# Performance work log

Measured on AMD Instinct MI355X. Metric: run time of the kernel, lower is better.

The kernel has to match this reference:

```python
import jax, jax.numpy as jnp
import numpy as np

# Constants from the source's eval path
BBOX_STDS = (0.1, 0.1, 0.2, 0.2)   # cfg.TRAIN.BBOX_NORMALIZE_STDS (MEANS are zeros)
PRE_NMS = 300                       # cfg.TEST.RPN_POST_NMS_TOP_N
POST_K = 100                        # cfg.PERSON_NMS (fixed output size; zero-padded)
NMS_THRESH = 0.3
SCORE_THRESH = 0.05


def setup_inputs() -> dict:
    key = jax.random.key(0)
    k1, k2, k3, k4 = jax.random.split(key, 4)
    B, N = 64, 32768
    H = W = 1024.0
    # plausible RPN proposal boxes inside the image
    xy = jax.random.uniform(k1, (B, N, 2)) * (W - 160.0)
    wh = jax.random.uniform(k2, (B, N, 2)) * 120.0 + 8.0
    boxes = jnp.concatenate([xy, xy + wh], axis=-1)          # [B,N,4] x1y1x2y2
    cls_prob = jax.random.uniform(k3, (B, N, 2))              # softmax probs [bg, person]
    box_deltas = jax.random.normal(k4, (B, N, 4)) * 0.5
    im_info = jnp.tile(jnp.array([H, W, 1.0], jnp.float32), (B, 1))
    return {"cls_prob": cls_prob, "boxes": boxes, "box_deltas": box_deltas, "im_info": im_info}


def _decode_and_clip(boxes, deltas, im_info):
    # bbox_transform_inv with de-normalized deltas, then clip_boxes
    stds = jnp.array(BBOX_STDS, boxes.dtype)
    d = deltas * stds                                         # MEANS are zero
    w = boxes[..., 2] - boxes[..., 0] + 1.0
    h = boxes[..., 3] - boxes[..., 1] + 1.0
    cx = boxes[..., 0] + 0.5 * w
    cy = boxes[..., 1] + 0.5 * h
    pcx = d[..., 0] * w + cx
    pcy = d[..., 1] * h + cy
    pw = jnp.exp(d[..., 2]) * w
    ph = jnp.exp(d[..., 3]) * h
    x1 = pcx - 0.5 * pw
    y1 = pcy - 0.5 * ph
    x2 = pcx + 0.5 * pw
    y2 = pcy + 0.5 * ph
    hmax = im_info[:, 0][:, None] - 1.0   # [B,1]
    wmax = im_info[:, 1][:, None] - 1.0
    x1 = jnp.clip(x1, 0.0, wmax)
    y1 = jnp.clip(y1, 0.0, hmax)
    x2 = jnp.clip(x2, 0.0, wmax)
    y2 = jnp.clip(y2, 0.0, hmax)
    return jnp.stack([x1, y1, x2, y2], axis=-1)               # [B,N,4]


def _nms_single(boxes_i, scores_i):
    # threshold -> sort (top-k) -> greedy NMS -> fixed-size padded output
    valid = scores_i >= SCORE_THRESH
    s = jnp.where(valid, scores_i, -jnp.inf)
    topv, topi = jax.lax.top_k(s, PRE_NMS)                    # descending sort + pre_nms_topN
    b = boxes_i[topi]                                          # [M,4]
    x1, y1, x2, y2 = b[:, 0], b[:, 1], b[:, 2], b[:, 3]
    areas = (x2 - x1 + 1.0) * (y2 - y1 + 1.0)
    xx1 = jnp.maximum(x1[:, None], x1[None, :])
    yy1 = jnp.maximum(y1[:, None], y1[None, :])
    xx2 = jnp.minimum(x2[:, None], x2[None, :])
    yy2 = jnp.minimum(y2[:, None], y2[None, :])
    inter = jnp.maximum(xx2 - xx1 + 1.0, 0.0) * jnp.maximum(yy2 - yy1 + 1.0, 0.0)
    iou = inter / (areas[:, None] + areas[None, :] - inter)    # [M,M]
    iou = jax.lax.stop_gradient(iou)                           # only drives the boolean keep mask
    idx = jnp.arange(PRE_NMS)
    keep0 = jnp.isfinite(topv)                                 # drop below-threshold padding

    def body(i, keep):
        sup = (iou[i] > NMS_THRESH) & (idx > i) & keep[i]
        return keep & ~sup

    keep = jax.lax.fori_loop(0, PRE_NMS, body, keep0)
    # compact kept boxes (in score order) into a fixed [POST_K,4] buffer, zero-padded
    rank = jnp.cumsum(keep) - 1
    dst = jnp.where(keep & (rank < POST_K), rank, POST_K)      # overflow row POST_K is discarded
    out = jnp.zeros((POST_K + 1, 4), b.dtype).at[dst].set(b)
    return out[:POST_K]


def reference(cls_prob, boxes, box_deltas, im_info):
    pred = _decode_and_clip(boxes, box_deltas, im_info)        # [B,N,4]
    scores_person = cls_prob[:, :, 1]                          # person column
    kept = jax.vmap(_nms_single)(pred, scores_person)          # [B,POST_K,4]
    B = pred.shape[0]
    bidx = jnp.broadcast_to(jnp.arange(B, dtype=pred.dtype)[:, None, None], (B, POST_K, 1))
    return jnp.concatenate([bidx, kept], axis=-1)              # [B,POST_K,5] rois
```

## Files before the change

kernel.cpp:

```cpp
#include <hip/hip_runtime.h>
#include <cstdint>
#include <cstddef>

#define PRE_NMS  300
#define POST_K   100
#define NBUCKET  4096
#define CAND_MAX 2048
#define NCHUNK   16
#define SUB      128
#define NWORDS   5
#define KCAP     192
#define KW       3
#define SUP_STRIDE 8
#define NBUK     512
#define MBASE    0xC0800000u
#define NMS_T    0.3f
#define SCORE_T  0.05f
#define FAST_T   0.9875f

typedef unsigned long long u64;

__global__ __launch_bounds__(256) void scan_kernel(
    const float* __restrict__ cls_prob,
    u64* __restrict__ candG,
    int* __restrict__ cntG,
    int N)
{
    const int b     = blockIdx.x >> 4;
    const int chunk = blockIdx.x & (NCHUNK - 1);
    const int nq    = N / 2;
    const int per   = (nq + NCHUNK - 1) / NCHUNK;
    const int base  = chunk * per;
    const int end   = min(base + per, nq);

    __shared__ int lcnt;
    __shared__ u64 lbuf[SUB];
    if (threadIdx.x == 0) lcnt = 0;
    __syncthreads();

    const float4* cp = (const float4*)(cls_prob + (size_t)b * N * 2);
    for (int q = base + threadIdx.x; q < end; q += 256) {
        float4 v = cp[q];
        #pragma unroll
        for (int h = 0; h < 2; ++h) {
            float s = h ? v.w : v.y;
            if (s >= FAST_T) {
                int pos = atomicAdd(&lcnt, 1);
                if (pos < SUB) {
                    unsigned int m = __float_as_uint(s) ^ 0xFFFFFFFFu;
                    lbuf[pos] = ((u64)m << 32) | (unsigned int)(2 * q + h);
                }
            }
        }
    }
    __syncthreads();

    const int cnt = lcnt;
    u64* cb = candG + ((size_t)b * NCHUNK + chunk) * SUB;
    for (int i = threadIdx.x; i < min(cnt, SUB); i += 256) cb[i] = lbuf[i];
    if (threadIdx.x == 0) cntG[b * NCHUNK + chunk] = cnt;
}

__device__ __forceinline__ u64 keep_init_word(int Kv, int w) {
    int rem = Kv - 64 * w;
    if (rem >= 64) return ~0ull;
    if (rem <= 0)  return 0ull;
    return (1ull << rem) - 1ull;
}

__device__ __forceinline__ u64 bits_above(int b) {
    return (b == 63) ? 0ull : (~0ull << (b + 1));
}

__device__ __forceinline__ int key_bucket(u64 key) {
    unsigned int m = (unsigned int)(key >> 32);
    int d = (int)(m - MBASE);
    if (d < 0) return 0;
    int bu = d >> 9;
    return (bu > NBUK - 1) ? (NBUK - 1) : bu;
}

__device__ __forceinline__ float box_area(float4 v) {
    return (v.z - v.x + 1.0f) * (v.w - v.y + 1.0f);
}

__global__ __launch_bounds__(512) void proposal_kernel(
    const float* __restrict__ cls_prob,
    const float* __restrict__ boxes,
    const float* __restrict__ deltas,
    const float* __restrict__ im_info,
    float* __restrict__ out,
    const u64* __restrict__ candG,
    const int* __restrict__ cntG,
    int useWS, int N)
{
    const int b   = blockIdx.x;
    const int tid = threadIdx.x;
    const int NT  = 512;

    __shared__ u64 cand[CAND_MAX];
    int* hist4k = (int*)cand;
    __shared__ float4 bb[PRE_NMS];
    int* buk_off = (int*)bb;
    int* buk_cnt = buk_off + NBUK;
    __shared__ u64 supRow[PRE_NMS * SUP_STRIDE];
    u64* skey2 = supRow;
    __shared__ u64 skey[PRE_NMS];
    __shared__ u64 keepw[NWORDS];
    __shared__ int sel[POST_K];
    __shared__ int ws8[8];
    __shared__ int n_out;
    __shared__ int need_full;
    __shared__ int sh_cc;
    __shared__ int sh_ok;
    __shared__ int cand_count;
    __shared__ int cutoff;
    __shared__ int ccnt[NCHUNK], coff[NCHUNK + 1];

    if (tid == 0) { cand_count = 0; need_full = 0; }
    __syncthreads();

    const float4* cp = (const float4*)(cls_prob + (size_t)b * N * 2);
    const int nq = N / 2;

    if (useWS && tid < NCHUNK) ccnt[tid] = cntG[b * NCHUNK + tid];
    __syncthreads();
    if (tid == 0) {
        int ok = useWS;
        int tot = 0;
        if (useWS) {
            for (int c = 0; c < NCHUNK; ++c) {
                if (ccnt[c] > SUB) ok = 0;
                coff[c] = tot;
                tot += ccnt[c];
            }
            coff[NCHUNK] = tot;
            if (tot < PRE_NMS || tot > CAND_MAX) ok = 0;
        }
        sh_ok = ok;
        sh_cc = tot;
    }
    __syncthreads();
    const bool fast = (sh_ok != 0);
    int cc;

    if (fast) {
        cc = sh_cc;
        const int c = tid >> 5;
        const u64* cb = candG + ((size_t)b * NCHUNK + c) * SUB;
        const int n = ccnt[c], o = coff[c];
        for (int i = tid & 31; i < n; i += 32) cand[o + i] = cb[i];
        __syncthreads();

        for (int i = tid; i < NBUK; i += NT) { buk_off[i] = 0; buk_cnt[i] = 0; }
        __syncthreads();
        for (int c2 = tid; c2 < cc; c2 += NT)
            atomicAdd(&buk_off[key_bucket(cand[c2])], 1);
        __syncthreads();
        {
            int v = buk_off[tid];
            int lane = tid & 63;
            int incl = v;
            #pragma unroll
            for (int d = 1; d < 64; d <<= 1) {
                int nv = __shfl_up(incl, d, 64);
                if (lane >= d) incl += nv;
            }
            if (lane == 63) ws8[tid >> 6] = incl;
            __syncthreads();
            int woff = 0;
            #pragma unroll
            for (int w = 0; w < 8; ++w)
                if (w < (tid >> 6)) woff += ws8[w];
            __syncthreads();
            buk_off[tid] = woff + incl - v;
        }
        __syncthreads();
        for (int c2 = tid; c2 < cc; c2 += NT) {
            u64 my = cand[c2];
            int bu = key_bucket(my);
            int slot = buk_off[bu] + atomicAdd(&buk_cnt[bu], 1);
            skey2[slot] = my;
        }
        __syncthreads();
        for (int s = tid; s < cc; s += NT) {
            u64 my = skey2[s];
            int bu = key_bucket(my);
            int o = buk_off[bu], n = buk_cnt[bu];
            int r = o;
            for (int t = o; t < o + n; ++t) r += (skey2[t] < my) ? 1 : 0;
            if (r < PRE_NMS) skey[r] = my;
        }
        __syncthreads();
    } else {
        for (int q = tid; q < nq; q += NT) {
            float4 v = cp[q];
            #pragma unroll
            for (int h = 0; h < 2; ++h) {
                float s = h ? v.w : v.y;
                if (s >= FAST_T) {
                    int pos = atomicAdd(&cand_count, 1);
                    if (pos < CAND_MAX) {
                        unsigned int m = __float_as_uint(s) ^ 0xFFFFFFFFu;
                        cand[pos] = ((u64)m << 32) | (unsigned int)(2 * q + h);
                    }
                }
            }
        }
        __syncthreads();
        if (cand_count < PRE_NMS) {
            for (int i = tid; i < NBUCKET; i += NT) hist4k[i] = 0;
            __syncthreads();
            for (int q = tid; q < nq; q += NT) {
                float4 v = cp[q];
                if (v.y >= SCORE_T) atomicAdd(&hist4k[min((int)(v.y * (float)NBUCKET), NBUCKET - 1)], 1);
                if (v.w >= SCORE_T) atomicAdd(&hist4k[min((int)(v.w * (float)NBUCKET), NBUCKET - 1)], 1);
            }
            __syncthreads();
            if (tid == 0) {
                int acc = 0, c = 0;
                for (int i = NBUCKET - 1; i >= 0; --i) {
                    acc += hist4k[i];
                    if (acc >= PRE_NMS) { c = i; break; }
                }
                cutoff = c;
                cand_count = 0;
            }
            __syncthreads();
            const int c = cutoff;
            for (int q = tid; q < nq; q += NT) {
                float4 v = cp[q];
                #pragma unroll
                for (int h = 0; h < 2; ++h) {
                    float s = h ? v.w : v.y;
                    if (s >= SCORE_T) {
                        int bu = min((int)(s * (float)NBUCKET), NBUCKET - 1);
                        if (bu >= c) {
                            int pos = atomicAdd(&cand_count, 1);
                            if (pos < CAND_MAX) {
                                unsigned int m = __float_as_uint(s) ^ 0xFFFFFFFFu;
                                cand[pos] = ((u64)m << 32) | (unsigned int)(2 * q + h);
                            }
                        }
                    }
                }
            }
            __syncthreads();
        }
        cc = min(cand_count, CAND_MAX);
        if (tid == 0) sh_cc = cc;
        __syncthreads();
        cc = sh_cc;
        for (int c2 = tid; c2 < cc; c2 += NT) {
            u64 my = cand[c2];
            int r = 0;
            for (int k = 0; k < cc; ++k) r += (cand[k] < my) ? 1 : 0;
            if (r < PRE_NMS) skey[r] = my;
        }
        __syncthreads();
    }

    const int Kv = min(cc, PRE_NMS);

    const float hmax = im_info[b * 3 + 0] - 1.0f;
    const float wmax = im_info[b * 3 + 1] - 1.0f;
    if (tid < PRE_NMS) {
        if (tid < Kv) {
            int idx = (int)(skey[tid] & 0xFFFFFFFFull);
            float4 bo = *(const float4*)(boxes  + ((size_t)b * N + idx) * 4);
            float4 de = *(const float4*)(deltas + ((size_t)b * N + idx) * 4);
            float w  = bo.z - bo.x + 1.0f;
            float hh = bo.w - bo.y + 1.0f;
            float cx = bo.x + 0.5f * w;
            float cy = bo.y + 0.5f * hh;
            float pcx = de.x * 0.1f * w + cx;
            float pcy = de.y * 0.1f * hh + cy;
            float pw  = expf(de.z * 0.2f) * w;
            float ph  = expf(de.w * 0.2f) * hh;
            float x1 = fminf(fmaxf(pcx - 0.5f * pw, 0.0f), wmax);
            float y1 = fminf(fmaxf(pcy - 0.5f * ph, 0.0f), hmax);
            float x2 = fminf(fmaxf(pcx + 0.5f * pw, 0.0f), wmax);
            float y2 = fminf(fmaxf(pcy + 0.5f * ph, 0.0f), hmax);
            bb[tid] = make_float4(x1, y1, x2, y2);
        } else {
            bb[tid] = make_float4(0.f, 0.f, 0.f, 0.f);
        }
    }
    __syncthreads();

    {
        const int lane = tid & 63;
        const int wv   = tid >> 6;
        float4 cb[KW]; float ca[KW];
        #pragma unroll
        for (int g = 0; g < KW; ++g) {
            float4 v = bb[g * 64 + lane];
            cb[g] = v;
            ca[g] = box_area(v);
        }
        for (int i = wv; i < KCAP; i += 8) {
            float4 bi = bb[i];
            float ai = box_area(bi);
            const int wi = i >> 6, bbit = i & 63;
            u64* rp = supRow + (size_t)i * SUP_STRIDE;
            #pragma unroll
            for (int g = 0; g < KW; ++g) {
                u64 word = 0;
                if (g >= wi) {
                    float xx1 = fmaxf(bi.x, cb[g].x);
                    float yy1 = fmaxf(bi.y, cb[g].y);
                    float xx2 = fminf(bi.z, cb[g].z);
                    float yy2 = fminf(bi.w, cb[g].w);
                    float iw = fmaxf(xx2 - xx1 + 1.0f, 0.0f);
                    float ih = fmaxf(yy2 - yy1 + 1.0f, 0.0f);
                    float inter = iw * ih;
                    bool ov = (inter > NMS_T * (ai + ca[g] - inter));
                    u64 bal = __ballot(ov);
                    word = (g == wi) ? (bal & bits_above(bbit)) : bal;
                }
                if (lane == 0) rp[g] = word;
            }
        }
    }
    __syncthreads();

    if (tid < 64) {
        u64 kw0 = keep_init_word(Kv, 0);
        u64 kw1 = keep_init_word(Kv, 1);
        u64 kw2 = keep_init_word(Kv, 2);

        int nk = 0;
        #pragma unroll
        for (int wi = 0; wi < KW; ++wi) {
            if (nk >= POST_K) break;
            u64 w = (wi == 0) ? kw0 : (wi == 1) ? kw1 : kw2;
            while (w != 0ull && nk < POST_K) {
                int b1 = __ffsll(w) - 1;
                u64 w1 = w & bits_above(b1);
                int b2 = (w1 != 0ull) ? (__ffsll(w1) - 1) : -1;
                u64 w2 = (b2 >= 0) ? (w1 & bits_above(b2)) : 0ull;
                int b3 = (w2 != 0ull) ? (__ffsll(w2) - 1) : -1;
                u64 w3 = (b3 >= 0) ? (w2 & bits_above(b3)) : 0ull;
                int b4 = (w3 != 0ull) ? (__ffsll(w3) - 1) : -1;

                const int base = wi * 64;
                const u64* p1 = supRow + (size_t)(base + b1) * SUP_STRIDE;
                const u64* p2 = supRow + (size_t)(base + ((b2 >= 0) ? b2 : b1)) * SUP_STRIDE;
                const u64* p3 = supRow + (size_t)(base + ((b3 >= 0) ? b3 : b1)) * SUP_STRIDE;
                const u64* p4 = supRow + (size_t)(base + ((b4 >= 0) ? b4 : b1)) * SUP_STRIDE;
                u64 a0 = p1[0], a1 = p1[1], a2 = p1[2];
                u64 c0 = p2[0], c1 = p2[1], c2 = p2[2];
                u64 d0 = p3[0], d1 = p3[1], d2 = p3[2];
                u64 e0 = p4[0], e1 = p4[1], e2 = p4[2];

                u64 aw = (wi == 0) ? a0 : (wi == 1) ? a1 : a2;
                u64 cw = (wi == 0) ? c0 : (wi == 1) ? c1 : c2;
                u64 dw = (wi == 0) ? d0 : (wi == 1) ? d1 : d2;

                kw0 &= ~a0; kw1 &= ~a1; kw2 &= ~a2;
                ++nk;
                bool k2 = false, k3 = false;
                if (b2 >= 0 && nk < POST_K && !((aw >> b2) & 1ull)) {
                    kw0 &= ~c0; kw1 &= ~c1; kw2 &= ~c2;
                    ++nk; k2 = true;
                }
                if (b3 >= 0 && nk < POST_K && !((aw >> b3) & 1ull)
                    && !(k2 && ((cw >> b3) & 1ull))) {
                    kw0 &= ~d0; kw1 &= ~d1; kw2 &= ~d2;
                    ++nk; k3 = true;
                }
                if (b4 >= 0 && nk < POST_K && !((aw >> b4) & 1ull)
                    && !(k2 && ((cw >> b4) & 1ull))
                    && !(k3 && ((dw >> b4) & 1ull))) {
                    kw0 &= ~e0; kw1 &= ~e1; kw2 &= ~e2;
                    ++nk;
                }
                int blast = (b4 >= 0) ? b4 : ((b3 >= 0) ? b3 : ((b2 >= 0) ? b2 : b1));
                u64 self = (wi == 0) ? kw0 : (wi == 1) ? kw1 : kw2;
                w = self & bits_above(blast);
            }
        }
        if (tid == 0) {
            keepw[0] = kw0; keepw[1] = kw1; keepw[2] = kw2;
            keepw[3] = 0ull; keepw[4] = 0ull;
            n_out = nk;
            need_full = (nk < POST_K && Kv > KCAP) ? 1 : 0;
        }
    }
    __syncthreads();

    if (need_full) {
        for (int t = tid; t < PRE_NMS * NWORDS; t += NT) {
            int w = t / PRE_NMS;
            int i = t - w * PRE_NMS;
            int jbase = w * 64;
            int jend  = min(jbase + 64, PRE_NMS);
            u64 bits = 0;
            int jstart = max(jbase, i + 1);
            if (jstart < jend) {
                float4 bi = bb[i];
                float ai = box_area(bi);
                for (int j = jstart; j < jend; ++j) {
                    float4 bj = bb[j];
                    float aj = box_area(bj);
                    float xx1 = fmaxf(bi.x, bj.x);
                    float yy1 = fmaxf(bi.y, bj.y);
                    float xx2 = fminf(bi.z, bj.z);
                    float yy2 = fminf(bi.w, bj.w);
                    float iw = fmaxf(xx2 - xx1 + 1.0f, 0.0f);
                    float ih = fmaxf(yy2 - yy1 + 1.0f, 0.0f);
                    float inter = iw * ih;
                    if (inter > NMS_T * (ai + aj - inter)) bits |= (1ull << (j - jbase));
                }
            }
            supRow[i * SUP_STRIDE + w] = bits;
        }
        __syncthreads();
        if (tid == 0) {
            u64 kk[NWORDS];
            #pragma unroll
            for (int w = 0; w < NWORDS; ++w) kk[w] = keep_init_word(Kv, w);
            int nk = 0;
            for (int i = 0; i < PRE_NMS && nk < POST_K; ++i) {
                if ((kk[i >> 6] >> (i & 63)) & 1ull) {
                    const u64* r = supRow + (size_t)i * SUP_STRIDE;
                    #pragma unroll
                    for (int w = 0; w < NWORDS; ++w) kk[w] &= ~r[w];
                    ++nk;
                }
            }
            #pragma unroll
            for (int w = 0; w < NWORDS; ++w) keepw[w] = kk[w];
            n_out = nk;
        }
        __syncthreads();
    }

    if (tid < PRE_NMS) {
        int wi = tid >> 6, bi = tid & 63;
        u64 w = keepw[wi];
        int prefix = 0;
        #pragma unroll
        for (int ww = 0; ww < NWORDS; ++ww)
            if (ww < wi) prefix += __popcll(keepw[ww]);
        prefix += __popcll(w & ((1ull << bi) - 1ull));
        if (((w >> bi) & 1ull) && prefix < POST_K) sel[prefix] = tid;
    }
    __syncthreads();

    if (tid < POST_K) {
        float* op = out + ((size_t)b * POST_K + tid) * 5;
        op[0] = (float)b;
        if (tid < n_out) {
            float4 v = bb[sel[tid]];
            op[1] = v.x; op[2] = v.y; op[3] = v.z; op[4] = v.w;
        } else {
            op[1] = 0.0f; op[2] = 0.0f; op[3] = 0.0f; op[4] = 0.0f;
        }
    }
}

extern "C" void kernel_launch(void* const* d_in, const int* in_sizes, int n_in,
                              void* d_out, int out_size, void* d_ws, size_t ws_size,
                              hipStream_t stream) {
    const float* cls_prob = (const float*)d_in[0];
    const float* boxes    = (const float*)d_in[1];
    const float* deltas   = (const float*)d_in[2];
    const float* im_info  = (const float*)d_in[3];
    float* out = (float*)d_out;

    const int B = in_sizes[3] / 3;
    const int N = in_sizes[0] / (B * 2);

    int* cntG   = (int*)d_ws;
    u64* candG  = (u64*)((char*)d_ws + 16384);
    size_t need = 16384 + (size_t)B * NCHUNK * SUB * sizeof(u64);
    int useWS   = (ws_size >= need && B * NCHUNK * (int)sizeof(int) <= 16384) ? 1 : 0;

    if (useWS) {
        scan_kernel<<<B * NCHUNK, 256, 0, stream>>>(cls_prob, candG, cntG, N);
    }
    proposal_kernel<<<B, 512, 0, stream>>>(cls_prob, boxes, deltas, im_info, out,
                                           candG, cntG, useWS, N);
}
```

Baseline: 125.2 us.

## Decode candidate boxes in scan kernel and place sorted boxes directly

Box gathering and decoding for candidates moves from the per-image proposal kernel, which runs with only 64 blocks, into the wide scan kernel. That kernel now writes decoded float4 boxes next to the sort keys in the workspace. The proposal kernel gives each candidate its own thread, buckets and ranks it, and writes its box straight into the sorted slot, removing the skey array, a staging copy and the separate serial gather/decode phase. In exchange, every candidate above the fast threshold is decoded even if it never makes the top 300, and the fast path now requires at most 512 candidates (one per thread).

```diff
diff --git a/kernel.cpp b/kernel.cpp
--- a/kernel.cpp
+++ b/kernel.cpp
@@ -20,9 +20,30 @@
 
 typedef unsigned long long u64;
 
+__device__ __forceinline__ float4 decode_box(float4 bo, float4 de,
+                                             float wmax, float hmax) {
+    float w  = bo.z - bo.x + 1.0f;
+    float hh = bo.w - bo.y + 1.0f;
+    float cx = bo.x + 0.5f * w;
+    float cy = bo.y + 0.5f * hh;
+    float pcx = de.x * 0.1f * w + cx;
+    float pcy = de.y * 0.1f * hh + cy;
+    float pw  = expf(de.z * 0.2f) * w;
+    float ph  = expf(de.w * 0.2f) * hh;
+    float x1 = fminf(fmaxf(pcx - 0.5f * pw, 0.0f), wmax);
+    float y1 = fminf(fmaxf(pcy - 0.5f * ph, 0.0f), hmax);
+    float x2 = fminf(fmaxf(pcx + 0.5f * pw, 0.0f), wmax);
+    float y2 = fminf(fmaxf(pcy + 0.5f * ph, 0.0f), hmax);
+    return make_float4(x1, y1, x2, y2);
+}
+
 __global__ __launch_bounds__(256) void scan_kernel(
     const float* __restrict__ cls_prob,
-    u64* __restrict__ candG,
+    const float* __restrict__ boxes,
+    const float* __restrict__ deltas,
+    const float* __restrict__ im_info,
+    u64* __restrict__ keyG,
+    float4* __restrict__ boxG,
     int* __restrict__ cntG,
     int N)
 {
@@ -34,10 +55,13 @@
     const int end   = min(base + per, nq);
 
     __shared__ int lcnt;
-    __shared__ u64 lbuf[SUB];
+    __shared__ u64 lk[SUB];
+    __shared__ float4 lb[SUB];
     if (threadIdx.x == 0) lcnt = 0;
     __syncthreads();
 
+    const float hmax = im_info[b * 3 + 0] - 1.0f;
+    const float wmax = im_info[b * 3 + 1] - 1.0f;
     const float4* cp = (const float4*)(cls_prob + (size_t)b * N * 2);
     for (int q = base + threadIdx.x; q < end; q += 256) {
         float4 v = cp[q];
@@ -47,8 +71,12 @@
             if (s >= FAST_T) {
                 int pos = atomicAdd(&lcnt, 1);
                 if (pos < SUB) {
+                    int idx = 2 * q + h;
                     unsigned int m = __float_as_uint(s) ^ 0xFFFFFFFFu;
-                    lbuf[pos] = ((u64)m << 32) | (unsigned int)(2 * q + h);
+                    float4 bo = *(const float4*)(boxes  + ((size_t)b * N + idx) * 4);
+                    float4 de = *(const float4*)(deltas + ((size_t)b * N + idx) * 4);
+                    lk[pos] = ((u64)m << 32) | (unsigned int)idx;
+                    lb[pos] = decode_box(bo, de, wmax, hmax);
                 }
             }
         }
@@ -56,9 +84,14 @@
     __syncthreads();
 
     const int cnt = lcnt;
-    u64* cb = candG + ((size_t)b * NCHUNK + chunk) * SUB;
-    for (int i = threadIdx.x; i < min(cnt, SUB); i += 256) cb[i] = lbuf[i];
-    if (threadIdx.x == 0) cntG[b * NCHUNK + chunk] = cnt;
+    const size_t obase = (size_t)b * NCHUNK + chunk;
+    u64* kb = keyG + obase * SUB;
+    float4* bbo = boxG + obase * SUB;
+    for (int i = threadIdx.x; i < min(cnt, SUB); i += 256) {
+        kb[i]  = lk[i];
+        bbo[i] = lb[i];
+    }
+    if (threadIdx.x == 0) cntG[obase] = cnt;
 }
 
 __device__ __forceinline__ u64 keep_init_word(int Kv, int w) {
@@ -90,7 +123,8 @@
     const float* __restrict__ deltas,
     const float* __restrict__ im_info,
     float* __restrict__ out,
-    const u64* __restrict__ candG,
+    const u64* __restrict__ keyG,
+    const float4* __restrict__ boxG,
     const int* __restrict__ cntG,
     int useWS, int N)
 {
@@ -100,12 +134,11 @@
 
     __shared__ u64 cand[CAND_MAX];
     int* hist4k = (int*)cand;
+    int* buk_off = (int*)cand;
+    int* buk_cnt = buk_off + NBUK;
     __shared__ float4 bb[PRE_NMS];
-    int* buk_off = (int*)bb;
-    int* buk_cnt = buk_off + NBUK;
     __shared__ u64 supRow[PRE_NMS * SUP_STRIDE];
     u64* skey2 = supRow;
-    __shared__ u64 skey[PRE_NMS];
     __shared__ u64 keepw[NWORDS];
     __shared__ int sel[POST_K];
     __shared__ int ws8[8];
@@ -122,6 +155,8 @@
 
     const float4* cp = (const float4*)(cls_prob + (size_t)b * N * 2);
     const int nq = N / 2;
+    const float hmax = im_info[b * 3 + 0] - 1.0f;
+    const float wmax = im_info[b * 3 + 1] - 1.0f;
 
     if (useWS && tid < NCHUNK) ccnt[tid] = cntG[b * NCHUNK + tid];
     __syncthreads();
@@ -135,7 +170,7 @@
                 tot += ccnt[c];
             }
             coff[NCHUNK] = tot;
-            if (tot < PRE_NMS || tot > CAND_MAX) ok = 0;
+            if (tot < PRE_NMS || tot > NT) ok = 0;
         }
         sh_ok = ok;
         sh_cc = tot;
@@ -146,16 +181,23 @@
 
     if (fast) {
         cc = sh_cc;
-        const int c = tid >> 5;
-        const u64* cb = candG + ((size_t)b * NCHUNK + c) * SUB;
-        const int n = ccnt[c], o = coff[c];
-        for (int i = tid & 31; i < n; i += 32) cand[o + i] = cb[i];
-        __syncthreads();
-
-        for (int i = tid; i < NBUK; i += NT) { buk_off[i] = 0; buk_cnt[i] = 0; }
-        __syncthreads();
-        for (int c2 = tid; c2 < cc; c2 += NT)
-            atomicAdd(&buk_off[key_bucket(cand[c2])], 1);
+        buk_off[tid] = 0;
+        buk_cnt[tid] = 0;
+        if (tid < PRE_NMS) bb[tid] = make_float4(0.f, 0.f, 0.f, 0.f);
+        __syncthreads();
+
+        const bool have = (tid < cc);
+        u64 my = 0; float4 mybox = make_float4(0.f, 0.f, 0.f, 0.f);
+        int bu = 0;
+        if (have) {
+            int ch = 0;
+            while (ch < NCHUNK - 1 && coff[ch + 1] <= tid) ++ch;
+            size_t p = ((size_t)b * NCHUNK + ch) * SUB + (tid - coff[ch]);
+            my = keyG[p];
+            mybox = boxG[p];
+            bu = key_bucket(my);
+            atomicAdd(&buk_off[bu], 1);
+        }
         __syncthreads();
         {
             int v = buk_off[tid];
@@ -176,20 +218,13 @@
             buk_off[tid] = woff + incl - v;
         }
         __syncthreads();
-        for (int c2 = tid; c2 < cc; c2 += NT) {
-            u64 my = cand[c2];
-            int bu = key_bucket(my);
-            int slot = buk_off[bu] + atomicAdd(&buk_cnt[bu], 1);
-            skey2[slot] = my;
-        }
-        __syncthreads();
-        for (int s = tid; s < cc; s += NT) {
-            u64 my = skey2[s];
-            int bu = key_bucket(my);
+        if (have) skey2[buk_off[bu] + atomicAdd(&buk_cnt[bu], 1)] = my;
+        __syncthreads();
+        if (have) {
             int o = buk_off[bu], n = buk_cnt[bu];
             int r = o;
             for (int t = o; t < o + n; ++t) r += (skey2[t] < my) ? 1 : 0;
-            if (r < PRE_NMS) skey[r] = my;
+            if (r < PRE_NMS) bb[r] = mybox;
         }
         __syncthreads();
     } else {
@@ -251,42 +286,23 @@
         if (tid == 0) sh_cc = cc;
         __syncthreads();
         cc = sh_cc;
+        if (tid < PRE_NMS) bb[tid] = make_float4(0.f, 0.f, 0.f, 0.f);
+        __syncthreads();
         for (int c2 = tid; c2 < cc; c2 += NT) {
             u64 my = cand[c2];
             int r = 0;
             for (int k = 0; k < cc; ++k) r += (cand[k] < my) ? 1 : 0;
-            if (r < PRE_NMS) skey[r] = my;
+            if (r < PRE_NMS) {
+                int idx = (int)(my & 0xFFFFFFFFull);
+                float4 bo = *(const float4*)(boxes  + ((size_t)b * N + idx) * 4);
+                float4 de = *(const float4*)(deltas + ((size_t)b * N + idx) * 4);
+                bb[r] = decode_box(bo, de, wmax, hmax);
+            }
         }
         __syncthreads();
     }
 
     const int Kv = min(cc, PRE_NMS);
-
-    const float hmax = im_info[b * 3 + 0] - 1.0f;
-    const float wmax = im_info[b * 3 + 1] - 1.0f;
-    if (tid < PRE_NMS) {
-        if (tid < Kv) {
-            int idx = (int)(skey[tid] & 0xFFFFFFFFull);
-            float4 bo = *(const float4*)(boxes  + ((size_t)b * N + idx) * 4);
-            float4 de = *(const float4*)(deltas + ((size_t)b * N + idx) * 4);
-            float w  = bo.z - bo.x + 1.0f;
-            float hh = bo.w - bo.y + 1.0f;
-            float cx = bo.x + 0.5f * w;
-            float cy = bo.y + 0.5f * hh;
-            float pcx = de.x * 0.1f * w + cx;
-            float pcy = de.y * 0.1f * hh + cy;
-            float pw  = expf(de.z * 0.2f) * w;
-            float ph  = expf(de.w * 0.2f) * hh;
-            float x1 = fminf(fmaxf(pcx - 0.5f * pw, 0.0f), wmax);
-            float y1 = fminf(fmaxf(pcy - 0.5f * ph, 0.0f), hmax);
-            float x2 = fminf(fmaxf(pcx + 0.5f * pw, 0.0f), wmax);
-            float y2 = fminf(fmaxf(pcy + 0.5f * ph, 0.0f), hmax);
-            bb[tid] = make_float4(x1, y1, x2, y2);
-        } else {
-            bb[tid] = make_float4(0.f, 0.f, 0.f, 0.f);
-        }
-    }
-    __syncthreads();
 
     {
         const int lane = tid & 63;
@@ -472,14 +488,17 @@
     const int B = in_sizes[3] / 3;
     const int N = in_sizes[0] / (B * 2);
 
-    int* cntG   = (int*)d_ws;
-    u64* candG  = (u64*)((char*)d_ws + 16384);
-    size_t need = 16384 + (size_t)B * NCHUNK * SUB * sizeof(u64);
+    const size_t nSlots = (size_t)B * NCHUNK * SUB;
+    int*    cntG = (int*)d_ws;
+    u64*    keyG = (u64*)((char*)d_ws + 16384);
+    float4* boxG = (float4*)((char*)d_ws + 16384 + nSlots * sizeof(u64));
+    size_t need = 16384 + nSlots * (sizeof(u64) + sizeof(float4));
     int useWS   = (ws_size >= need && B * NCHUNK * (int)sizeof(int) <= 16384) ? 1 : 0;
 
     if (useWS) {
-        scan_kernel<<<B * NCHUNK, 256, 0, stream>>>(cls_prob, candG, cntG, N);
+        scan_kernel<<<B * NCHUNK, 256, 0, stream>>>(cls_prob, boxes, deltas, im_info,
+                                                    keyG, boxG, cntG, N);
     }
     proposal_kernel<<<B, 512, 0, stream>>>(cls_prob, boxes, deltas, im_info, out,
-                                           candG, cntG, useWS, N);
-}
+                                           keyG, boxG, cntG, useWS, N);
+}
```

Result: no change. 127.5 us (+1.8%).
